# Performance work log

Measured on AMD Instinct MI355X. Metric: run time of the kernel, lower is better.

The kernel has to match this reference:

```python
import jax, jax.numpy as jnp
import numpy as np

N = 100000   # occupied voxels
C = 128      # input_dim
G = 64       # voxel grid extent per axis


def _build_neighbor_map(rng):
    # random unique voxel coords in a G^3 grid + hash lookup for 3x3x3 offsets
    lin = rng.choice(G ** 3, size=N, replace=False)
    coords = np.stack(np.unravel_index(lin, (G, G, G)), axis=1).astype(np.int64)  # [N,3]
    lut = np.full(G ** 3, -1, np.int32)
    lut[lin] = np.arange(N, dtype=np.int32)
    o = np.arange(-1, 2)
    offs = np.stack(np.meshgrid(o, o, o, indexing='ij'), -1).reshape(27, 3)  # [27,3]
    nc = coords[None, :, :] + offs[:, None, :]                 # [27,N,3]
    valid = ((nc >= 0) & (nc < G)).all(-1)                     # [27,N]
    nlin = (nc[..., 0] * G + nc[..., 1]) * G + nc[..., 2]
    nbr = np.where(valid, lut[np.clip(nlin, 0, G ** 3 - 1)], -1).astype(np.int32)
    return nbr


def setup_inputs() -> dict:
    rng = np.random.default_rng(0)
    nbr = _build_neighbor_map(rng)
    key = jax.random.key(0)
    ks = jax.random.split(key, 5)
    h = C // 2
    x = jax.random.normal(ks[0], (N, C), jnp.float32)
    w1 = jax.random.normal(ks[1], (C, C), jnp.float32) * 0.05
    b1 = jnp.zeros((C,), jnp.float32)
    w2 = jax.random.normal(ks[2], (C, C), jnp.float32) * 0.05
    b2 = jnp.zeros((C,), jnp.float32)
    rw1 = jax.random.normal(ks[3], (27, h, h), jnp.float32) * 0.05
    rb1 = jnp.zeros((h,), jnp.float32)
    rw2 = jax.random.normal(ks[4], (27, h, h), jnp.float32) * 0.05
    rb2 = jnp.zeros((h,), jnp.float32)
    return dict(x=x, w1=w1, b1=b1, w2=w2, b2=b2,
                rw1=rw1, rb1=rb1, rw2=rw2, rb2=rb2,
                nbr=jnp.asarray(nbr))


def _sconv3(feat, nbr, W, b):
    # sparse 3x3x3 conv: gather neighbor features per kernel offset, GEMM, sum
    mask = (nbr >= 0).astype(feat.dtype)                  # [27,N]
    g = feat[jnp.maximum(nbr, 0)] * mask[:, :, None]      # [27,N,c]
    return jnp.einsum('knc,kcd->nd', g, W) + b            # [N,c]


def reference(x, w1, b1, w2, b2, rw1, rb1, rw2, rb2, nbr):
    h = x.shape[1] // 2
    y = x @ w1 + b1                                       # conv1 (1x1x1)
    conv_x, trans_x = y[:, :h], y[:, h:]                  # split
    # resblock (stride 1 -> no skip conv): relu(conv)->relu(conv) + identity
    r = jax.nn.relu(_sconv3(conv_x, nbr, rw1, rb1))
    r = jax.nn.relu(_sconv3(r, nbr, rw2, rb2))
    conv_x = (r + conv_x) + conv_x                        # resblock(x) + x
    # CodedVTRBlock source unavailable: modeled as identity on trans branch
    res = jnp.concatenate([conv_x, trans_x], axis=1) @ w2 + b2  # conv2 (1x1x1)
    return x + res
```

## Files before the change

### kernel.cpp

```cpp
#include <hip/hip_runtime.h>


#define N_PTS 100000
#define NBLK64 1563
#define NBLK128 782

typedef __attribute__((ext_vector_type(8))) short frag_ab;
typedef __attribute__((ext_vector_type(4))) float f32x4;
#define ZFRAG frag_ab{0, 0, 0, 0, 0, 0, 0, 0}

__device__ __forceinline__ unsigned short f2bf(float f) {
  union { float f; unsigned int i; } v; v.f = f;
  unsigned int r = v.i + 0x7fffu + ((v.i >> 16) & 1u);
  return (unsigned short)(r >> 16);
}
__device__ __forceinline__ float bf2f(unsigned short u) {
  union { unsigned int i; float f; } v; v.i = ((unsigned int)u) << 16; return v.f;
}

__device__ __forceinline__ void gload_lds16(const unsigned short* g, unsigned short* l) {
  __builtin_amdgcn_global_load_lds(
      (const __attribute__((address_space(1))) unsigned int*)g,
      (__attribute__((address_space(3))) unsigned int*)(unsigned int)(size_t)l,
      16, 0, 0);
}

__global__ __launch_bounds__(256) void k_prep(
    const float* __restrict__ w1, const float* __restrict__ w2,
    const float* __restrict__ rw1, const float* __restrict__ rw2,
    unsigned short* __restrict__ w1T, unsigned short* __restrict__ w2T,
    unsigned short* __restrict__ rw1T, unsigned short* __restrict__ rw2T) {
  int t = blockIdx.x * 256 + threadIdx.x;
  if (t < 128 * 128) {
    int c = t >> 7, d = t & 127;
    int pos = d * 128 + ((((c >> 3) ^ (d & 15)) << 3) | (c & 7));
    w1T[pos] = f2bf(w1[t]);
    w2T[pos] = f2bf(w2[t]);
  }
  if (t < 27 * 64 * 64) {
    int k = t >> 12, r = t & 4095, c = r >> 6, d = r & 63;
    int pos = (k << 12) + d * 64 + ((((c >> 3) ^ (d & 7)) << 3) | (c & 7));
    rw1T[pos] = f2bf(rw1[t]);
    rw2T[pos] = f2bf(rw2[t]);
  }
}

__global__ __launch_bounds__(256) void k_gemm_in(
    const float* __restrict__ x, const unsigned short* __restrict__ w1T,
    const float* __restrict__ b1, unsigned short* __restrict__ y) {
  __shared__ unsigned short sw[16384];
  const int tid = threadIdx.x, lane = tid & 63, w = tid >> 6;
  const int m16 = lane & 15, q = lane >> 4;
#pragma unroll
  for (int r = 0; r < 8; ++r) {
    const int off = (w * 8 + r) * 512 + lane * 8;
    gload_lds16(w1T + off, &sw[off]);
  }
  __syncthreads();
  const int rowbase = blockIdx.x * 64 + w * 16;
  const int r0 = rowbase + m16;
  const int rc = r0 < N_PTS ? r0 : N_PTS - 1;
  f32x4 acc[8] = {};
#pragma unroll
  for (int kk = 0; kk < 4; ++kk) {
    const float* xp = x + (size_t)rc * 128 + kk * 32 + q * 8;
    float4 f0 = *(const float4*)xp;
    float4 f1 = *(const float4*)(xp + 4);
    frag_ab a;
    a[0] = (short)f2bf(f0.x); a[1] = (short)f2bf(f0.y);
    a[2] = (short)f2bf(f0.z); a[3] = (short)f2bf(f0.w);
    a[4] = (short)f2bf(f1.x); a[5] = (short)f2bf(f1.y);
    a[6] = (short)f2bf(f1.z); a[7] = (short)f2bf(f1.w);
#pragma unroll
    for (int ct = 0; ct < 8; ++ct) {
      const int d = ct * 16 + m16;
      const int phys = ((kk << 2) | q) ^ m16;
      frag_ab bf = *(const frag_ab*)(&sw[d * 128 + phys * 8]);
      acc[ct] = __builtin_amdgcn_mfma_f32_16x16x32_bf16(a, bf, acc[ct], 0, 0, 0);
    }
  }
#pragma unroll
  for (int ct = 0; ct < 8; ++ct) {
    const int col = ct * 16 + m16;
    const float bias = b1[col];
#pragma unroll
    for (int j = 0; j < 4; ++j) {
      int r = rowbase + q * 4 + j;
      if (r < N_PTS) y[(size_t)r * 128 + col] = f2bf(acc[ct][j] + bias);
    }
  }
}

template <bool FUSE>
__global__ __launch_bounds__(256) void k_conv(
    const unsigned short* __restrict__ feat, const int fstride,
    const int* __restrict__ nbr,
    const unsigned short* __restrict__ rwT, const float* __restrict__ rb,
    const unsigned short* __restrict__ res, unsigned short* __restrict__ out) {
  __shared__ unsigned short sw[4][4096];
  const int tid = threadIdx.x, lane = tid & 63, w = tid >> 6;
  const int m16 = lane & 15, q = lane >> 4;
  const int rowbase = blockIdx.x * 128 + w * 32;
  const int p0 = rowbase + m16, p1 = p0 + 16;
  const bool v0 = p0 < N_PTS, v1 = p1 < N_PTS;
  const int pc0 = v0 ? p0 : N_PTS - 1, pc1 = v1 ? p1 : N_PTS - 1;
  const int s0 = w * 1024 + lane * 8;
  const int s1 = s0 + 512;

  int I[4][2];
  int im[2][2];
  frag_ab A[2][2][2];
  f32x4 acc[2][4] = {};

#define CONV_GATHER(slot, isrc)                                                 \
  {                                                                             \
    const int i0 = v0 ? (isrc)[0] : -1;                                         \
    const int i1 = v1 ? (isrc)[1] : -1;                                         \
    im[slot][0] = i0; im[slot][1] = i1;                                         \
    const size_t j0 = (size_t)(i0 < 0 ? 0 : i0);                                \
    const size_t j1 = (size_t)(i1 < 0 ? 0 : i1);                                \
    const unsigned short* f0 = feat + j0 * fstride + q * 8;                     \
    const unsigned short* f1 = feat + j1 * fstride + q * 8;                     \
    A[slot][0][0] = *(const frag_ab*)f0; A[slot][0][1] = *(const frag_ab*)(f0 + 32); \
    A[slot][1][0] = *(const frag_ab*)f1; A[slot][1][1] = *(const frag_ab*)(f1 + 32); \
  }

#define CONV_COMPUTE(buf, slot)                                                 \
  {                                                                             \
    frag_ab Ac[2][2];                                                           \
    _Pragma("unroll") for (int rt = 0; rt < 2; ++rt)                            \
      _Pragma("unroll") for (int kk = 0; kk < 2; ++kk) {                        \
        frag_ab a = A[slot][rt][kk];                                            \
        if (im[slot][rt] < 0) a = ZFRAG;                                        \
        Ac[rt][kk] = a;                                                         \
      }                                                                         \
    _Pragma("unroll") for (int kk = 0; kk < 2; ++kk)                            \
      _Pragma("unroll") for (int ct = 0; ct < 4; ++ct) {                        \
        const int d = ct * 16 + m16;                                            \
        const int phys = ((kk << 2) | q) ^ (m16 & 7);                           \
        frag_ab bf = *(const frag_ab*)(&sw[buf][d * 64 + phys * 8]);            \
        acc[0][ct] = __builtin_amdgcn_mfma_f32_16x16x32_bf16(Ac[0][kk], bf, acc[0][ct], 0, 0, 0); \
        acc[1][ct] = __builtin_amdgcn_mfma_f32_16x16x32_bf16(Ac[1][kk], bf, acc[1][ct], 0, 0, 0); \
      }                                                                         \
  }

  gload_lds16(rwT + s0, &sw[0][s0]);
  gload_lds16(rwT + s1, &sw[0][s1]);
  gload_lds16(rwT + 4096 + s0, &sw[1][s0]);
  gload_lds16(rwT + 4096 + s1, &sw[1][s1]);
#pragma unroll
  for (int s = 0; s < 3; ++s) {
    I[s][0] = nbr[(size_t)s * N_PTS + pc0];
    I[s][1] = nbr[(size_t)s * N_PTS + pc1];
  }
  CONV_GATHER(0, I[0]);
  __builtin_amdgcn_s_barrier();

  for (int k0 = 0; k0 < 24; k0 += 4) {
#pragma unroll
    for (int u = 0; u < 4; ++u) {
      const int k = k0 + u;
      const int cur = u & 1, nxt = cur ^ 1;
      {
        const unsigned short* src = rwT + ((size_t)(k + 2) << 12);
        unsigned short* dst = sw[(u + 2) & 3];
        gload_lds16(src + s0, dst + s0);
        gload_lds16(src + s1, dst + s1);
      }
      I[(u + 3) & 3][0] = nbr[(size_t)(k + 3) * N_PTS + pc0];
      I[(u + 3) & 3][1] = nbr[(size_t)(k + 3) * N_PTS + pc1];
      CONV_GATHER(nxt, I[(u + 1) & 3]);
      asm volatile("s_waitcnt vmcnt(8)" ::: "memory");
      __builtin_amdgcn_sched_barrier(0);
      CONV_COMPUTE(u & 3, cur);
      __builtin_amdgcn_s_barrier();
    }
  }

  {
    const unsigned short* src = rwT + ((size_t)26 << 12);
    gload_lds16(src + s0, &sw[2][s0]);
    gload_lds16(src + s1, &sw[2][s1]);
    CONV_GATHER(1, I[1]);
    asm volatile("s_waitcnt vmcnt(6)" ::: "memory");
    __builtin_amdgcn_sched_barrier(0);
    CONV_COMPUTE(0, 0);
    __builtin_amdgcn_s_barrier();
  }
  {
    CONV_GATHER(0, I[2]);
    asm volatile("s_waitcnt vmcnt(4)" ::: "memory");
    __builtin_amdgcn_sched_barrier(0);
    CONV_COMPUTE(1, 1);
    __builtin_amdgcn_s_barrier();
  }
  {
    asm volatile("s_waitcnt vmcnt(0)" ::: "memory");
    __builtin_amdgcn_sched_barrier(0);
    CONV_COMPUTE(2, 0);
  }
#undef CONV_GATHER
#undef CONV_COMPUTE

#pragma unroll
  for (int ct = 0; ct < 4; ++ct) {
    const int col = ct * 16 + m16;
    const float bias = rb[col];
#pragma unroll
    for (int rt = 0; rt < 2; ++rt)
#pragma unroll
      for (int j = 0; j < 4; ++j) {
        const int r = rowbase + rt * 16 + q * 4 + j;
        if (r < N_PTS) {
          float v = acc[rt][ct][j] + bias;
          v = v > 0.f ? v : 0.f;
          if constexpr (FUSE) v += 2.f * bf2f(res[(size_t)r * 128 + col]);
          out[(size_t)r * 64 + col] = f2bf(v);
        }
      }
  }
}

__global__ __launch_bounds__(256) void k_gemm_out(
    const float* __restrict__ x, const unsigned short* __restrict__ z1,
    const unsigned short* __restrict__ y, const unsigned short* __restrict__ w2T,
    const float* __restrict__ b2, float* __restrict__ out) {
  __shared__ unsigned short sw[16384];
  const int tid = threadIdx.x, lane = tid & 63, w = tid >> 6;
  const int m16 = lane & 15, q = lane >> 4;
#pragma unroll
  for (int r = 0; r < 8; ++r) {
    const int off = (w * 8 + r) * 512 + lane * 8;
    gload_lds16(w2T + off, &sw[off]);
  }
  __syncthreads();
  const int rowbase = blockIdx.x * 64 + w * 16;
  const int r0 = rowbase + m16;
  const int rc = r0 < N_PTS ? r0 : N_PTS - 1;
  f32x4 acc[8] = {};
#pragma unroll
  for (int kk = 0; kk < 4; ++kk) {
    const unsigned short* ap = (kk < 2)
        ? (z1 + (size_t)rc * 64 + kk * 32 + q * 8)
        : (y + (size_t)rc * 128 + 64 + (kk - 2) * 32 + q * 8);
    frag_ab a = *(const frag_ab*)ap;
#pragma unroll
    for (int ct = 0; ct < 8; ++ct) {
      const int d = ct * 16 + m16;
      const int phys = ((kk << 2) | q) ^ m16;
      frag_ab bf = *(const frag_ab*)(&sw[d * 128 + phys * 8]);
      acc[ct] = __builtin_amdgcn_mfma_f32_16x16x32_bf16(a, bf, acc[ct], 0, 0, 0);
    }
  }
#pragma unroll
  for (int ct = 0; ct < 8; ++ct) {
    const int col = ct * 16 + m16;
    const float bias = b2[col];
#pragma unroll
    for (int j = 0; j < 4; ++j) {
      int r = rowbase + q * 4 + j;
      if (r < N_PTS) {
        size_t o = (size_t)r * 128 + col;
        out[o] = acc[ct][j] + bias + x[o];
      }
    }
  }
}

extern "C" void kernel_launch(void* const* d_in, const int* in_sizes, int n_in,
                              void* d_out, int out_size, void* d_ws, size_t ws_size,
                              hipStream_t stream) {
  const float* x   = (const float*)d_in[0];
  const float* w1  = (const float*)d_in[1];
  const float* b1  = (const float*)d_in[2];
  const float* w2  = (const float*)d_in[3];
  const float* b2  = (const float*)d_in[4];
  const float* rw1 = (const float*)d_in[5];
  const float* rb1 = (const float*)d_in[6];
  const float* rw2 = (const float*)d_in[7];
  const float* rb2 = (const float*)d_in[8];
  const int* nbr = (const int*)d_in[9];
  float* out = (float*)d_out;

  char* ws = (char*)d_ws;
  unsigned short* w1T  = (unsigned short*)(ws);
  unsigned short* w2T  = (unsigned short*)(ws + 32768);
  unsigned short* rw1T = (unsigned short*)(ws + 65536);
  unsigned short* rw2T = (unsigned short*)(ws + 286720);
  unsigned short* y    = (unsigned short*)(ws + 507904);
  unsigned short* r1   = (unsigned short*)(ws + 507904 + 25600000);
  unsigned short* z1   = (unsigned short*)(ws + 507904 + 38400000);

  k_prep<<<432, 256, 0, stream>>>(w1, w2, rw1, rw2, w1T, w2T, rw1T, rw2T);
  k_gemm_in<<<NBLK64, 256, 0, stream>>>(x, w1T, b1, y);
  k_conv<false><<<NBLK128, 256, 0, stream>>>(y, 128, nbr, rw1T, rb1, nullptr, r1);
  k_conv<true><<<NBLK128, 256, 0, stream>>>(r1, 64, nbr, rw2T, rb2, y, z1);
  k_gemm_out<<<NBLK64, 256, 0, stream>>>(x, z1, y, w2T, b2, out);
}
```

Measured before the change: 275.3 us.

## Load conv weights directly into registers with one-wave blocks, dropping LDS staging

The sparse conv kernel now runs one 64-thread wave per block handling 32 points, and each wave loads the per-offset weight fragments straight from global memory (L2/L1) into registers with double buffering, replacing the shared-memory ring buffer, async LDS loads and barriers. The weight layout loses its XOR swizzle since there is no LDS bank conflict to avoid. Bounds checks are removed because N is a multiple of 32. This trades barrier and LDS traffic for redundant global weight reads per wave, since weights are no longer shared across four waves, plus higher register pressure.

```diff
diff --git a/kernel.cpp b/kernel.cpp
--- a/kernel.cpp
+++ b/kernel.cpp
@@ -3,6 +3,7 @@
 
 #define N_PTS 100000
 #define NBLK64 1563
+#define NBLK32 3125
 #define NBLK128 782
 
 typedef __attribute__((ext_vector_type(8))) short frag_ab;
@@ -39,7 +40,7 @@
   }
   if (t < 27 * 64 * 64) {
     int k = t >> 12, r = t & 4095, c = r >> 6, d = r & 63;
-    int pos = (k << 12) + d * 64 + ((((c >> 3) ^ (d & 7)) << 3) | (c & 7));
+    int pos = (k << 12) + d * 64 + c;
     rw1T[pos] = f2bf(rw1[t]);
     rw2T[pos] = f2bf(rw2[t]);
   }
@@ -92,30 +93,38 @@
 }
 
 template <bool FUSE>
-__global__ __launch_bounds__(256) void k_conv(
+__global__ __launch_bounds__(64, 3) void k_conv(
     const unsigned short* __restrict__ feat, const int fstride,
     const int* __restrict__ nbr,
     const unsigned short* __restrict__ rwT, const float* __restrict__ rb,
     const unsigned short* __restrict__ res, unsigned short* __restrict__ out) {
-  __shared__ unsigned short sw[4][4096];
-  const int tid = threadIdx.x, lane = tid & 63, w = tid >> 6;
+  const int lane = threadIdx.x & 63;
   const int m16 = lane & 15, q = lane >> 4;
-  const int rowbase = blockIdx.x * 128 + w * 32;
+  const int rowbase = blockIdx.x * 32;
   const int p0 = rowbase + m16, p1 = p0 + 16;
-  const bool v0 = p0 < N_PTS, v1 = p1 < N_PTS;
-  const int pc0 = v0 ? p0 : N_PTS - 1, pc1 = v1 ? p1 : N_PTS - 1;
-  const int s0 = w * 1024 + lane * 8;
-  const int s1 = s0 + 512;
 
   int I[4][2];
   int im[2][2];
   frag_ab A[2][2][2];
+  frag_ab B[2][4][2];
   f32x4 acc[2][4] = {};
+
+#define CONV_LOADI(s, kidx)                                                     \
+  {                                                                             \
+    I[s][0] = nbr[(size_t)(kidx) * N_PTS + p0];                                 \
+    I[s][1] = nbr[(size_t)(kidx) * N_PTS + p1];                                 \
+  }
+
+#define CONV_LOADB(slot, kidx)                                                  \
+  _Pragma("unroll") for (int ct = 0; ct < 4; ++ct)                              \
+    _Pragma("unroll") for (int kk = 0; kk < 2; ++kk)                            \
+      B[slot][ct][kk] = *(const frag_ab*)(rwT + ((size_t)(kidx) << 12) +        \
+                                          (ct * 16 + m16) * 64 + kk * 32 + q * 8);
 
 #define CONV_GATHER(slot, isrc)                                                 \
   {                                                                             \
-    const int i0 = v0 ? (isrc)[0] : -1;                                         \
-    const int i1 = v1 ? (isrc)[1] : -1;                                         \
+    const int i0 = (isrc)[0];                                                   \
+    const int i1 = (isrc)[1];                                                   \
     im[slot][0] = i0; im[slot][1] = i1;                                         \
     const size_t j0 = (size_t)(i0 < 0 ? 0 : i0);                                \
     const size_t j1 = (size_t)(i1 < 0 ? 0 : i1);                                \
@@ -125,7 +134,7 @@
     A[slot][1][0] = *(const frag_ab*)f1; A[slot][1][1] = *(const frag_ab*)(f1 + 32); \
   }
 
-#define CONV_COMPUTE(buf, slot)                                                 \
+#define CONV_COMPUTE(slot)                                                      \
   {                                                                             \
     frag_ab Ac[2][2];                                                           \
     _Pragma("unroll") for (int rt = 0; rt < 2; ++rt)                            \
@@ -136,69 +145,38 @@
       }                                                                         \
     _Pragma("unroll") for (int kk = 0; kk < 2; ++kk)                            \
       _Pragma("unroll") for (int ct = 0; ct < 4; ++ct) {                        \
-        const int d = ct * 16 + m16;                                            \
-        const int phys = ((kk << 2) | q) ^ (m16 & 7);                           \
-        frag_ab bf = *(const frag_ab*)(&sw[buf][d * 64 + phys * 8]);            \
-        acc[0][ct] = __builtin_amdgcn_mfma_f32_16x16x32_bf16(Ac[0][kk], bf, acc[0][ct], 0, 0, 0); \
-        acc[1][ct] = __builtin_amdgcn_mfma_f32_16x16x32_bf16(Ac[1][kk], bf, acc[1][ct], 0, 0, 0); \
+        acc[0][ct] = __builtin_amdgcn_mfma_f32_16x16x32_bf16(Ac[0][kk], B[slot][ct][kk], acc[0][ct], 0, 0, 0); \
+        acc[1][ct] = __builtin_amdgcn_mfma_f32_16x16x32_bf16(Ac[1][kk], B[slot][ct][kk], acc[1][ct], 0, 0, 0); \
       }                                                                         \
   }
 
-  gload_lds16(rwT + s0, &sw[0][s0]);
-  gload_lds16(rwT + s1, &sw[0][s1]);
-  gload_lds16(rwT + 4096 + s0, &sw[1][s0]);
-  gload_lds16(rwT + 4096 + s1, &sw[1][s1]);
-#pragma unroll
-  for (int s = 0; s < 3; ++s) {
-    I[s][0] = nbr[(size_t)s * N_PTS + pc0];
-    I[s][1] = nbr[(size_t)s * N_PTS + pc1];
-  }
+  CONV_LOADI(0, 0);
+  CONV_LOADI(1, 1);
+  CONV_LOADI(2, 2);
+  CONV_LOADB(0, 0);
   CONV_GATHER(0, I[0]);
-  __builtin_amdgcn_s_barrier();
 
   for (int k0 = 0; k0 < 24; k0 += 4) {
 #pragma unroll
     for (int u = 0; u < 4; ++u) {
       const int k = k0 + u;
-      const int cur = u & 1, nxt = cur ^ 1;
-      {
-        const unsigned short* src = rwT + ((size_t)(k + 2) << 12);
-        unsigned short* dst = sw[(u + 2) & 3];
-        gload_lds16(src + s0, dst + s0);
-        gload_lds16(src + s1, dst + s1);
-      }
-      I[(u + 3) & 3][0] = nbr[(size_t)(k + 3) * N_PTS + pc0];
-      I[(u + 3) & 3][1] = nbr[(size_t)(k + 3) * N_PTS + pc1];
-      CONV_GATHER(nxt, I[(u + 1) & 3]);
-      asm volatile("s_waitcnt vmcnt(8)" ::: "memory");
-      __builtin_amdgcn_sched_barrier(0);
-      CONV_COMPUTE(u & 3, cur);
-      __builtin_amdgcn_s_barrier();
-    }
-  }
-
-  {
-    const unsigned short* src = rwT + ((size_t)26 << 12);
-    gload_lds16(src + s0, &sw[2][s0]);
-    gload_lds16(src + s1, &sw[2][s1]);
-    CONV_GATHER(1, I[1]);
-    asm volatile("s_waitcnt vmcnt(6)" ::: "memory");
-    __builtin_amdgcn_sched_barrier(0);
-    CONV_COMPUTE(0, 0);
-    __builtin_amdgcn_s_barrier();
-  }
-  {
-    CONV_GATHER(0, I[2]);
-    asm volatile("s_waitcnt vmcnt(4)" ::: "memory");
-    __builtin_amdgcn_sched_barrier(0);
-    CONV_COMPUTE(1, 1);
-    __builtin_amdgcn_s_barrier();
-  }
-  {
-    asm volatile("s_waitcnt vmcnt(0)" ::: "memory");
-    __builtin_amdgcn_sched_barrier(0);
-    CONV_COMPUTE(2, 0);
-  }
+      CONV_LOADI((u + 3) & 3, k + 3);
+      CONV_LOADB((u + 1) & 1, k + 1);
+      CONV_GATHER((u + 1) & 1, I[(u + 1) & 3]);
+      CONV_COMPUTE(u & 1);
+    }
+  }
+
+  CONV_LOADB(1, 25);
+  CONV_GATHER(1, I[1]);
+  CONV_COMPUTE(0);
+  CONV_LOADB(0, 26);
+  CONV_GATHER(0, I[2]);
+  CONV_COMPUTE(1);
+  CONV_COMPUTE(0);
+
+#undef CONV_LOADI
+#undef CONV_LOADB
 #undef CONV_GATHER
 #undef CONV_COMPUTE
 
@@ -211,12 +189,10 @@
 #pragma unroll
       for (int j = 0; j < 4; ++j) {
         const int r = rowbase + rt * 16 + q * 4 + j;
-        if (r < N_PTS) {
-          float v = acc[rt][ct][j] + bias;
-          v = v > 0.f ? v : 0.f;
-          if constexpr (FUSE) v += 2.f * bf2f(res[(size_t)r * 128 + col]);
-          out[(size_t)r * 64 + col] = f2bf(v);
-        }
+        float v = acc[rt][ct][j] + bias;
+        v = v > 0.f ? v : 0.f;
+        if constexpr (FUSE) v += 2.f * bf2f(res[(size_t)r * 128 + col]);
+        out[(size_t)r * 64 + col] = f2bf(v);
       }
   }
 }
@@ -293,7 +269,7 @@
 
   k_prep<<<432, 256, 0, stream>>>(w1, w2, rw1, rw2, w1T, w2T, rw1T, rw2T);
   k_gemm_in<<<NBLK64, 256, 0, stream>>>(x, w1T, b1, y);
-  k_conv<false><<<NBLK128, 256, 0, stream>>>(y, 128, nbr, rw1T, rb1, nullptr, r1);
-  k_conv<true><<<NBLK128, 256, 0, stream>>>(r1, 64, nbr, rw2T, rb2, y, z1);
+  k_conv<false><<<NBLK32, 64, 0, stream>>>(y, 128, nbr, rw1T, rb1, nullptr, r1);
+  k_conv<true><<<NBLK32, 64, 0, stream>>>(r1, 64, nbr, rw2T, rb2, y, z1);
   k_gemm_out<<<NBLK64, 256, 0, stream>>>(x, z1, y, w2T, b2, out);
 }
```

New measurement: 401.0 us. 45.6% more time.

## Stage neighbor indices in LDS and deepen gather/weight prefetch pipeline

Applied to the files above, without the earlier changes.

The conv kernel now loads all 27x128 neighbor indices for the block into shared memory up front instead of issuing scalar-per-lane global loads inside the loop. The feature gather and weight-tile prefetch are deepened from a 2-stage to a 3/4-stage ring (4 A-fragment slots, weights prefetched 3 offsets ahead), with looser vmcnt waits and no sched_barriers. This aims to hide more gather latency at the cost of more VGPRs and extra LDS (about 13.5KB), which may reduce occupancy. The vmcnt counts must match the issued loads exactly, or the kernel will read stale data.

```diff
diff --git a/kernel.cpp b/kernel.cpp
--- a/kernel.cpp
+++ b/kernel.cpp
@@ -98,47 +98,52 @@
     const unsigned short* __restrict__ rwT, const float* __restrict__ rb,
     const unsigned short* __restrict__ res, unsigned short* __restrict__ out) {
   __shared__ unsigned short sw[4][4096];
+  __shared__ int isl[27 * 128];
   const int tid = threadIdx.x, lane = tid & 63, w = tid >> 6;
   const int m16 = lane & 15, q = lane >> 4;
   const int rowbase = blockIdx.x * 128 + w * 32;
-  const int p0 = rowbase + m16, p1 = p0 + 16;
-  const bool v0 = p0 < N_PTS, v1 = p1 < N_PTS;
-  const int pc0 = v0 ? p0 : N_PTS - 1, pc1 = v1 ? p1 : N_PTS - 1;
   const int s0 = w * 1024 + lane * 8;
   const int s1 = s0 + 512;
-
-  int I[4][2];
-  int im[2][2];
-  frag_ab A[2][2][2];
+  const int ibase = w * 32 + m16;
+
+  for (int i = tid; i < 27 * 128; i += 256) {
+    const int kk = i >> 7, r = i & 127;
+    const int row = blockIdx.x * 128 + r;
+    isl[i] = (row < N_PTS) ? nbr[(size_t)kk * N_PTS + row] : -1;
+  }
+  __syncthreads();
+
+  int Ireg[2][2];
+  int im[4][2];
+  frag_ab A[4][2][2];
   f32x4 acc[2][4] = {};
 
-#define CONV_GATHER(slot, isrc)                                                 \
+#define CONV_GATHER(aslot, i0v, i1v)                                            \
   {                                                                             \
-    const int i0 = v0 ? (isrc)[0] : -1;                                         \
-    const int i1 = v1 ? (isrc)[1] : -1;                                         \
-    im[slot][0] = i0; im[slot][1] = i1;                                         \
-    const size_t j0 = (size_t)(i0 < 0 ? 0 : i0);                                \
-    const size_t j1 = (size_t)(i1 < 0 ? 0 : i1);                                \
+    const int gi0 = (i0v), gi1 = (i1v);                                         \
+    im[aslot][0] = gi0; im[aslot][1] = gi1;                                     \
+    const size_t j0 = (size_t)(gi0 < 0 ? 0 : gi0);                              \
+    const size_t j1 = (size_t)(gi1 < 0 ? 0 : gi1);                              \
     const unsigned short* f0 = feat + j0 * fstride + q * 8;                     \
     const unsigned short* f1 = feat + j1 * fstride + q * 8;                     \
-    A[slot][0][0] = *(const frag_ab*)f0; A[slot][0][1] = *(const frag_ab*)(f0 + 32); \
-    A[slot][1][0] = *(const frag_ab*)f1; A[slot][1][1] = *(const frag_ab*)(f1 + 32); \
-  }
-
-#define CONV_COMPUTE(buf, slot)                                                 \
+    A[aslot][0][0] = *(const frag_ab*)f0; A[aslot][0][1] = *(const frag_ab*)(f0 + 32); \
+    A[aslot][1][0] = *(const frag_ab*)f1; A[aslot][1][1] = *(const frag_ab*)(f1 + 32); \
+  }
+
+#define CONV_COMPUTE(bslot, aslot)                                              \
   {                                                                             \
     frag_ab Ac[2][2];                                                           \
     _Pragma("unroll") for (int rt = 0; rt < 2; ++rt)                            \
       _Pragma("unroll") for (int kk = 0; kk < 2; ++kk) {                        \
-        frag_ab a = A[slot][rt][kk];                                            \
-        if (im[slot][rt] < 0) a = ZFRAG;                                        \
+        frag_ab a = A[aslot][rt][kk];                                           \
+        if (im[aslot][rt] < 0) a = ZFRAG;                                       \
         Ac[rt][kk] = a;                                                         \
       }                                                                         \
     _Pragma("unroll") for (int kk = 0; kk < 2; ++kk)                            \
       _Pragma("unroll") for (int ct = 0; ct < 4; ++ct) {                        \
         const int d = ct * 16 + m16;                                            \
         const int phys = ((kk << 2) | q) ^ (m16 & 7);                           \
-        frag_ab bf = *(const frag_ab*)(&sw[buf][d * 64 + phys * 8]);            \
+        frag_ab bf = *(const frag_ab*)(&sw[bslot][d * 64 + phys * 8]);          \
         acc[0][ct] = __builtin_amdgcn_mfma_f32_16x16x32_bf16(Ac[0][kk], bf, acc[0][ct], 0, 0, 0); \
         acc[1][ct] = __builtin_amdgcn_mfma_f32_16x16x32_bf16(Ac[1][kk], bf, acc[1][ct], 0, 0, 0); \
       }                                                                         \
@@ -148,56 +153,48 @@
   gload_lds16(rwT + s1, &sw[0][s1]);
   gload_lds16(rwT + 4096 + s0, &sw[1][s0]);
   gload_lds16(rwT + 4096 + s1, &sw[1][s1]);
-#pragma unroll
-  for (int s = 0; s < 3; ++s) {
-    I[s][0] = nbr[(size_t)s * N_PTS + pc0];
-    I[s][1] = nbr[(size_t)s * N_PTS + pc1];
-  }
-  CONV_GATHER(0, I[0]);
+  gload_lds16(rwT + 8192 + s0, &sw[2][s0]);
+  gload_lds16(rwT + 8192 + s1, &sw[2][s1]);
+  Ireg[0][0] = isl[2 * 128 + ibase];
+  Ireg[0][1] = isl[2 * 128 + ibase + 16];
+  CONV_GATHER(0, isl[0 * 128 + ibase], isl[0 * 128 + ibase + 16]);
+  CONV_GATHER(1, isl[1 * 128 + ibase], isl[1 * 128 + ibase + 16]);
+  asm volatile("s_waitcnt vmcnt(8)" ::: "memory");
   __builtin_amdgcn_s_barrier();
 
   for (int k0 = 0; k0 < 24; k0 += 4) {
 #pragma unroll
     for (int u = 0; u < 4; ++u) {
       const int k = k0 + u;
-      const int cur = u & 1, nxt = cur ^ 1;
+      Ireg[(u + 3) & 1][0] = isl[(k + 3) * 128 + ibase];
+      Ireg[(u + 3) & 1][1] = isl[(k + 3) * 128 + ibase + 16];
       {
-        const unsigned short* src = rwT + ((size_t)(k + 2) << 12);
-        unsigned short* dst = sw[(u + 2) & 3];
+        const unsigned short* src = rwT + ((size_t)(k + 3) << 12);
+        unsigned short* dst = &sw[(u + 3) & 3][0];
         gload_lds16(src + s0, dst + s0);
         gload_lds16(src + s1, dst + s1);
       }
-      I[(u + 3) & 3][0] = nbr[(size_t)(k + 3) * N_PTS + pc0];
-      I[(u + 3) & 3][1] = nbr[(size_t)(k + 3) * N_PTS + pc1];
-      CONV_GATHER(nxt, I[(u + 1) & 3]);
-      asm volatile("s_waitcnt vmcnt(8)" ::: "memory");
-      __builtin_amdgcn_sched_barrier(0);
-      CONV_COMPUTE(u & 3, cur);
+      CONV_GATHER((u + 2) & 3, Ireg[(u + 2) & 1][0], Ireg[(u + 2) & 1][1]);
+      asm volatile("s_waitcnt vmcnt(12)" ::: "memory");
+      CONV_COMPUTE(u & 3, u & 3);
       __builtin_amdgcn_s_barrier();
     }
   }
 
   {
-    const unsigned short* src = rwT + ((size_t)26 << 12);
-    gload_lds16(src + s0, &sw[2][s0]);
-    gload_lds16(src + s1, &sw[2][s1]);
-    CONV_GATHER(1, I[1]);
-    asm volatile("s_waitcnt vmcnt(6)" ::: "memory");
-    __builtin_amdgcn_sched_barrier(0);
+    CONV_GATHER(2, Ireg[0][0], Ireg[0][1]);
+    asm volatile("s_waitcnt vmcnt(10)" ::: "memory");
     CONV_COMPUTE(0, 0);
     __builtin_amdgcn_s_barrier();
   }
   {
-    CONV_GATHER(0, I[2]);
     asm volatile("s_waitcnt vmcnt(4)" ::: "memory");
-    __builtin_amdgcn_sched_barrier(0);
     CONV_COMPUTE(1, 1);
     __builtin_amdgcn_s_barrier();
   }
   {
     asm volatile("s_waitcnt vmcnt(0)" ::: "memory");
-    __builtin_amdgcn_sched_barrier(0);
-    CONV_COMPUTE(2, 0);
+    CONV_COMPUTE(2, 2);
   }
 #undef CONV_GATHER
 #undef CONV_COMPUTE
```

After: 290.4 us. 1.05x slower.
